# Kernel tuning notes

Hardware: AMD Instinct MI355X
Metric: run time of the kernel (lower is better)

Reference implementation:

```python
import jax, jax.numpy as jnp
import numpy as np

B, T, C = 8, 2048, 1024
HS, HO = 64, 64  # head_size, head_output_dim

def setup_inputs() -> dict:
    key = jax.random.key(0)
    k1, k2, k3, k4 = jax.random.split(key, 4)
    x = jax.random.normal(k1, (B, T, C), dtype=jnp.float32)
    Wk = jax.random.normal(k2, (HS, C), dtype=jnp.float32) * (C ** -0.5)
    Wq = jax.random.normal(k3, (HS, C), dtype=jnp.float32) * (C ** -0.5)
    Wv = jax.random.normal(k4, (HO, C), dtype=jnp.float32) * (C ** -0.5)
    return {"x": x, "Wk": Wk, "Wq": Wq, "Wv": Wv}

def reference(x, Wk, Wq, Wv):
    Bx, Tx, Cx = x.shape
    k = jnp.einsum('btc,hc->bth', x, Wk)  # [B,T,HS]
    q = jnp.einsum('btc,hc->bth', x, Wq)  # [B,T,HS]
    v = jnp.einsum('btc,oc->bto', x, Wv)  # [B,T,HO]
    scores = jnp.einsum('bth,bsh->bts', q, k)  # [B,T,T]
    causal = jnp.tril(jnp.ones((Tx, Tx), dtype=bool))
    scores = jnp.where(causal, scores, -jnp.inf)
    # original scales AFTER masking; -inf * scale stays -inf, same softmax result
    weights = jax.nn.softmax(scores * (HS ** -0.5), axis=-1)
    return jnp.einsum('bts,bso->bto', weights, v)
```

## Files before the change

### kernel.cpp

```cpp
#include <hip/hip_runtime.h>
#include <hip/hip_bf16.h>

typedef __attribute__((ext_vector_type(8))) short short8;
typedef __attribute__((ext_vector_type(4))) float float4v;

#define LOG2E 1.44269504088896340736f

typedef __attribute__((address_space(1))) const unsigned int gu32;
typedef __attribute__((address_space(3))) unsigned int su32;

__device__ __forceinline__ unsigned short f2bf(float f) {
    unsigned int u = __float_as_uint(f);
    unsigned int r = (u + 0x7fffu + ((u >> 16) & 1u)) >> 16;
    return (unsigned short)r;
}

__global__ void wconv_kernel(const float* __restrict__ Wk, const float* __restrict__ Wq,
                             const float* __restrict__ Wv, unsigned short* __restrict__ Wb) {
    int i = blockIdx.x * 256 + threadIdx.x;
    if (i >= 192 * 1024) return;
    float v;
    if (i < 65536)       v = Wk[i];
    else if (i < 131072) v = Wq[i - 65536];
    else                 v = Wv[i - 131072];
    Wb[i] = f2bf(v);
}

__global__ __launch_bounds__(256) void proj_kernel(
    const float* __restrict__ x, const unsigned short* __restrict__ Wb,
    unsigned short* __restrict__ qs, unsigned short* __restrict__ ks,
    unsigned short* __restrict__ vT) {
    __shared__ unsigned short Bl[2][12288];

    const int tid  = threadIdx.x;
    const int lane = tid & 63;
    const int wave = tid >> 6;
    const int rg   = wave & 1;
    const int g    = wave >> 1;
    const int quad = lane >> 4;
    const int l16  = lane & 15;
    const int t0   = blockIdx.x * 32;

    const int srow_in = lane >> 3;
    const int csrc    = (lane & 7) ^ srow_in;

    const int rowA = t0 + rg * 16 + l16;
    const float* xr = x + (size_t)rowA * 1024;

    float4v acc[6];
#pragma unroll
    for (int n = 0; n < 6; n++) acc[n] = (float4v){0.f, 0.f, 0.f, 0.f};

#define STAGE_B(BUF, KN)                                                          \
    {                                                                             \
        _Pragma("unroll")                                                         \
        for (int i = 0; i < 6; i++) {                                             \
            const int region = wave * 6 + i;                                      \
            const int rowg   = region * 8 + srow_in;                              \
            const unsigned short* src = Wb + (size_t)rowg * 1024 + (KN) + csrc * 8; \
            __builtin_amdgcn_global_load_lds((gu32*)src,                          \
                                             (su32*)&Bl[BUF][region * 512],       \
                                             16, 0, 0);                           \
        }                                                                         \
    }

    STAGE_B(0, 0)
    float4v areg[4];
    areg[0] = *(const float4v*)(xr + quad * 8);
    areg[1] = *(const float4v*)(xr + quad * 8 + 4);
    areg[2] = *(const float4v*)(xr + 32 + quad * 8);
    areg[3] = *(const float4v*)(xr + 32 + quad * 8 + 4);

    const int swz = l16 & 7;

#pragma unroll 2
    for (int kt = 0; kt < 16; kt++) {
        __syncthreads();
        const int kn = ((kt + 1) & 15) * 64;
        STAGE_B((kt + 1) & 1, kn)
        float4v anext[4];
        anext[0] = *(const float4v*)(xr + kn + quad * 8);
        anext[1] = *(const float4v*)(xr + kn + quad * 8 + 4);
        anext[2] = *(const float4v*)(xr + kn + 32 + quad * 8);
        anext[3] = *(const float4v*)(xr + kn + 32 + quad * 8 + 4);
        const unsigned short* Bc = Bl[kt & 1];
#pragma unroll
        for (int kc = 0; kc < 2; kc++) {
            short8 af;
#pragma unroll
            for (int j = 0; j < 4; j++) af[j] = (short)f2bf(areg[kc * 2][j]);
#pragma unroll
            for (int j = 0; j < 4; j++) af[4 + j] = (short)f2bf(areg[kc * 2 + 1][j]);
#pragma unroll
            for (int n = 0; n < 6; n++) {
                const int row  = (g * 6 + n) * 16 + l16;
                const int coff = ((kc * 4 + quad) ^ swz) * 8;
                const short8 bf = *(const short8*)&Bc[row * 64 + coff];
                acc[n] = __builtin_amdgcn_mfma_f32_16x16x32_bf16(af, bf, acc[n], 0, 0, 0);
            }
        }
#pragma unroll
        for (int i = 0; i < 4; i++) areg[i] = anext[i];
    }
#undef STAGE_B

    const int rowD = t0 + rg * 16 + quad * 4;
#pragma unroll
    for (int r = 0; r < 4; r++) {
        const int t = rowD + r;
        const int b = t >> 11, tt = t & 2047;
        if (g == 0) {
#pragma unroll
            for (int n = 0; n < 4; n++)
                ks[(size_t)t * 64 + n * 16 + l16] = f2bf(acc[n][r]);
#pragma unroll
            for (int n = 4; n < 6; n++)
                qs[(size_t)t * 64 + (n - 4) * 16 + l16] = f2bf(acc[n][r] * 0.125f);
        } else {
#pragma unroll
            for (int n = 0; n < 2; n++)
                qs[(size_t)t * 64 + (n + 2) * 16 + l16] = f2bf(acc[n][r] * 0.125f);
#pragma unroll
            for (int n = 2; n < 6; n++)
                vT[(size_t)b * 131072 + (size_t)((n - 2) * 16 + l16) * 2048 + tt] = f2bf(acc[n][r]);
        }
    }
}

__global__ __launch_bounds__(256) void attn_kernel(
    const unsigned short* __restrict__ qs, const unsigned short* __restrict__ ks,
    const unsigned short* __restrict__ vT, float* __restrict__ out) {
    __shared__ unsigned short Kl[4 * 64 * 72];
    __shared__ unsigned short Vl[64 * 264];
    __shared__ unsigned short P[4][16 * 72];
    __shared__ float Ll[4][16];
    float* Of = (float*)Kl;

    const int tid  = threadIdx.x;
    const int lane = tid & 63;
    const int wave = tid >> 6;
    const int quad = lane >> 4;
    const int l16  = lane & 15;
    const int bx   = blockIdx.x;
    const int b    = bx & 7;
    const int i    = bx >> 3;
    const int qt   = (i & 1) ? (127 - (i >> 1)) : (i >> 1);
    const int t0   = qt * 16;

    const unsigned short* qb = qs + (size_t)b * 131072;
    const unsigned short* kb = ks + (size_t)b * 131072;
    const unsigned short* vb = vT + (size_t)b * 131072;

    const int ksr = tid >> 3;
    const int ksc = (tid & 7) * 8;
    const int vsr = tid >> 5;
    const int vsc = (tid & 31) * 8;

    const int qrow = t0 + l16;
    const short8 qf0 = *(const short8*)(qb + (size_t)qrow * 64 + quad * 8);
    const short8 qf1 = *(const short8*)(qb + (size_t)qrow * 64 + 32 + quad * 8);

    float4v o[4];
#pragma unroll
    for (int ot = 0; ot < 4; ot++) o[ot] = (float4v){0.f, 0.f, 0.f, 0.f};
    float lpart = 0.f;

    const int nkb  = (qt >> 2) + 1;
    const int nsup = (nkb + 3) >> 2;

    for (int s = 0; s < nsup; s++) {
        const int key0 = s * 256;
        __syncthreads();
#pragma unroll
        for (int i2 = 0; i2 < 8; i2++) {
            int kr = key0 + i2 * 32 + ksr; kr = kr < 2047 ? kr : 2047;
            *(short8*)&Kl[(i2 * 32 + ksr) * 72 + ksc] = *(const short8*)(kb + (size_t)kr * 64 + ksc);
        }
#pragma unroll
        for (int i2 = 0; i2 < 8; i2++) {
            const int orow = i2 * 8 + vsr;
            int kc2 = key0 + vsc; kc2 = kc2 < 2040 ? kc2 : 2040;
            *(short8*)&Vl[orow * 264 + vsc] = *(const short8*)(vb + (size_t)orow * 2048 + kc2);
        }
        __syncthreads();

        const int jt = s * 4 + wave;
        if (jt < nkb) {
            const int kbase = wave * 64;
            float4v sv[4];
#pragma unroll
            for (int kt = 0; kt < 4; kt++) {
                const short8 ka = *(const short8*)&Kl[(kbase + kt * 16 + l16) * 72 + quad * 8];
                const short8 kc = *(const short8*)&Kl[(kbase + kt * 16 + l16) * 72 + 32 + quad * 8];
                float4v z = (float4v){0.f, 0.f, 0.f, 0.f};
                z = __builtin_amdgcn_mfma_f32_16x16x32_bf16(ka, qf0, z, 0, 0, 0);
                sv[kt] = __builtin_amdgcn_mfma_f32_16x16x32_bf16(kc, qf1, z, 0, 0, 0);
            }
            if (jt == nkb - 1) {
#pragma unroll
                for (int kt = 0; kt < 4; kt++)
#pragma unroll
                    for (int r = 0; r < 4; r++)
                        if (jt * 64 + kt * 16 + quad * 4 + r > qrow) sv[kt][r] = -1e30f;
            }
#pragma unroll
            for (int kt = 0; kt < 4; kt++) {
                float p0 = exp2f(sv[kt][0] * LOG2E);
                float p1 = exp2f(sv[kt][1] * LOG2E);
                float p2 = exp2f(sv[kt][2] * LOG2E);
                float p3 = exp2f(sv[kt][3] * LOG2E);
                lpart += (p0 + p1) + (p2 + p3);
                unsigned int lo = (unsigned int)f2bf(p0) | ((unsigned int)f2bf(p1) << 16);
                unsigned int hi = (unsigned int)f2bf(p2) | ((unsigned int)f2bf(p3) << 16);
                unsigned long long w = ((unsigned long long)hi << 32) | lo;
                *(unsigned long long*)&P[wave][l16 * 72 + kt * 16 + quad * 4] = w;
            }
#pragma unroll
            for (int kc = 0; kc < 2; kc++) {
                const short8 pf = *(const short8*)&P[wave][l16 * 72 + kc * 32 + quad * 8];
#pragma unroll
                for (int ot = 0; ot < 4; ot++) {
                    const short8 vf = *(const short8*)&Vl[(ot * 16 + l16) * 264 + wave * 64 + kc * 32 + quad * 8];
                    o[ot] = __builtin_amdgcn_mfma_f32_16x16x32_bf16(pf, vf, o[ot], 0, 0, 0);
                }
            }
        }
    }

    lpart += __shfl_xor(lpart, 16);
    lpart += __shfl_xor(lpart, 32);
    __syncthreads();
#pragma unroll
    for (int r = 0; r < 4; r++)
#pragma unroll
        for (int ot = 0; ot < 4; ot++)
            Of[wave * 1088 + (quad * 4 + r) * 68 + ot * 16 + l16] = o[ot][r];
    if (lane < 16) Ll[wave][lane] = lpart;
    __syncthreads();

    {
        const int row = tid >> 4;
        const int c0  = (tid & 15) * 4;
        const float lsum = Ll[0][row] + Ll[1][row] + Ll[2][row] + Ll[3][row];
        float4v v0 = *(const float4v*)&Of[0 * 1088 + row * 68 + c0];
        float4v v1 = *(const float4v*)&Of[1 * 1088 + row * 68 + c0];
        float4v v2 = *(const float4v*)&Of[2 * 1088 + row * 68 + c0];
        float4v v3 = *(const float4v*)&Of[3 * 1088 + row * 68 + c0];
        float4v res;
        const float inv = 1.0f / lsum;
#pragma unroll
        for (int j = 0; j < 4; j++)
            res[j] = ((v0[j] + v1[j]) + (v2[j] + v3[j])) * inv;
        float* ob = out + (size_t)b * 131072 + (size_t)(t0 + row) * 64 + c0;
        *(float4v*)ob = res;
    }
}

extern "C" void kernel_launch(void* const* d_in, const int* in_sizes, int n_in,
                              void* d_out, int out_size, void* d_ws, size_t ws_size,
                              hipStream_t stream) {
    const float* x  = (const float*)d_in[0];
    const float* Wk = (const float*)d_in[1];
    const float* Wq = (const float*)d_in[2];
    const float* Wv = (const float*)d_in[3];
    float* out = (float*)d_out;

    unsigned short* Wb  = (unsigned short*)d_ws;
    unsigned short* qsb = (unsigned short*)((char*)d_ws + 393216);
    unsigned short* ksb = qsb + 1048576;
    unsigned short* vTb = ksb + 1048576;

    hipLaunchKernelGGL(wconv_kernel, dim3(768), dim3(256), 0, stream, Wk, Wq, Wv, Wb);
    hipLaunchKernelGGL(proj_kernel, dim3(512), dim3(256), 0, stream, x, Wb, qsb, ksb, vTb);
    hipLaunchKernelGGL(attn_kernel, dim3(1024), dim3(256), 0, stream, qsb, ksb, vTb, out);
}
```

Baseline: 152.7 us.

## Drop LDS staging in projection kernel, load weights directly from global

Rewrites the QKV projection kernel so each block handles 16 rows instead of 32 and each wave reads its three weight tiles straight from global memory (L2-resident) rather than staging them through double-buffered LDS with barriers. It also deepens x prefetching to two k-steps ahead and doubles the grid to 1024 blocks with a launch-bounds occupancy hint. The aim is to remove __syncthreads and LDS traffic and to raise occupancy. The cost is more global/L2 weight reads, because the weights are re-read by twice as many blocks and are no longer shared across waves through LDS.

```diff
diff --git a/kernel.cpp b/kernel.cpp
--- a/kernel.cpp
+++ b/kernel.cpp
@@ -5,9 +5,6 @@
 typedef __attribute__((ext_vector_type(4))) float float4v;
 
 #define LOG2E 1.44269504088896340736f
-
-typedef __attribute__((address_space(1))) const unsigned int gu32;
-typedef __attribute__((address_space(3))) unsigned int su32;
 
 __device__ __forceinline__ unsigned short f2bf(float f) {
     unsigned int u = __float_as_uint(f);
@@ -26,103 +23,97 @@
     Wb[i] = f2bf(v);
 }
 
-__global__ __launch_bounds__(256) void proj_kernel(
+__global__ __launch_bounds__(256, 4) void proj_kernel(
     const float* __restrict__ x, const unsigned short* __restrict__ Wb,
     unsigned short* __restrict__ qs, unsigned short* __restrict__ ks,
     unsigned short* __restrict__ vT) {
-    __shared__ unsigned short Bl[2][12288];
-
     const int tid  = threadIdx.x;
     const int lane = tid & 63;
     const int wave = tid >> 6;
-    const int rg   = wave & 1;
-    const int g    = wave >> 1;
     const int quad = lane >> 4;
     const int l16  = lane & 15;
-    const int t0   = blockIdx.x * 32;
-
-    const int srow_in = lane >> 3;
-    const int csrc    = (lane & 7) ^ srow_in;
-
-    const int rowA = t0 + rg * 16 + l16;
-    const float* xr = x + (size_t)rowA * 1024;
-
-    float4v acc[6];
-#pragma unroll
-    for (int n = 0; n < 6; n++) acc[n] = (float4v){0.f, 0.f, 0.f, 0.f};
-
-#define STAGE_B(BUF, KN)                                                          \
-    {                                                                             \
-        _Pragma("unroll")                                                         \
-        for (int i = 0; i < 6; i++) {                                             \
-            const int region = wave * 6 + i;                                      \
-            const int rowg   = region * 8 + srow_in;                              \
-            const unsigned short* src = Wb + (size_t)rowg * 1024 + (KN) + csrc * 8; \
-            __builtin_amdgcn_global_load_lds((gu32*)src,                          \
-                                             (su32*)&Bl[BUF][region * 512],       \
-                                             16, 0, 0);                           \
-        }                                                                         \
-    }
-
-    STAGE_B(0, 0)
-    float4v areg[4];
-    areg[0] = *(const float4v*)(xr + quad * 8);
-    areg[1] = *(const float4v*)(xr + quad * 8 + 4);
-    areg[2] = *(const float4v*)(xr + 32 + quad * 8);
-    areg[3] = *(const float4v*)(xr + 32 + quad * 8 + 4);
-
-    const int swz = l16 & 7;
+    const int t0   = blockIdx.x * 16;
+
+    const float* xr = x + (size_t)(t0 + l16) * 1024;
+
+    const unsigned short* brow0 = Wb + (size_t)((wave * 3 + 0) * 16 + l16) * 1024 + quad * 8;
+    const unsigned short* brow1 = brow0 + 16 * 1024;
+    const unsigned short* brow2 = brow0 + 32 * 1024;
+
+    float4v acc0 = (float4v){0.f, 0.f, 0.f, 0.f};
+    float4v acc1 = (float4v){0.f, 0.f, 0.f, 0.f};
+    float4v acc2 = (float4v){0.f, 0.f, 0.f, 0.f};
+
+    float4v a0[4], a1[4];
+    a0[0] = *(const float4v*)(xr + quad * 8);
+    a0[1] = *(const float4v*)(xr + quad * 8 + 4);
+    a0[2] = *(const float4v*)(xr + 32 + quad * 8);
+    a0[3] = *(const float4v*)(xr + 32 + quad * 8 + 4);
+    a1[0] = *(const float4v*)(xr + 64 + quad * 8);
+    a1[1] = *(const float4v*)(xr + 64 + quad * 8 + 4);
+    a1[2] = *(const float4v*)(xr + 96 + quad * 8);
+    a1[3] = *(const float4v*)(xr + 96 + quad * 8 + 4);
 
 #pragma unroll 2
     for (int kt = 0; kt < 16; kt++) {
-        __syncthreads();
-        const int kn = ((kt + 1) & 15) * 64;
-        STAGE_B((kt + 1) & 1, kn)
-        float4v anext[4];
-        anext[0] = *(const float4v*)(xr + kn + quad * 8);
-        anext[1] = *(const float4v*)(xr + kn + quad * 8 + 4);
-        anext[2] = *(const float4v*)(xr + kn + 32 + quad * 8);
-        anext[3] = *(const float4v*)(xr + kn + 32 + quad * 8 + 4);
-        const unsigned short* Bc = Bl[kt & 1];
-#pragma unroll
-        for (int kc = 0; kc < 2; kc++) {
+        const int kn = ((kt + 2) & 15) * 64;
+        float4v an[4];
+        an[0] = *(const float4v*)(xr + kn + quad * 8);
+        an[1] = *(const float4v*)(xr + kn + quad * 8 + 4);
+        an[2] = *(const float4v*)(xr + kn + 32 + quad * 8);
+        an[3] = *(const float4v*)(xr + kn + 32 + quad * 8 + 4);
+
+        const unsigned short* b0 = brow0 + kt * 64;
+        const unsigned short* b1 = brow1 + kt * 64;
+        const unsigned short* b2 = brow2 + kt * 64;
+        const short8 bf00 = *(const short8*)(b0);
+        const short8 bf01 = *(const short8*)(b1);
+        const short8 bf02 = *(const short8*)(b2);
+        const short8 bf10 = *(const short8*)(b0 + 32);
+        const short8 bf11 = *(const short8*)(b1 + 32);
+        const short8 bf12 = *(const short8*)(b2 + 32);
+
+        {
             short8 af;
 #pragma unroll
-            for (int j = 0; j < 4; j++) af[j] = (short)f2bf(areg[kc * 2][j]);
-#pragma unroll
-            for (int j = 0; j < 4; j++) af[4 + j] = (short)f2bf(areg[kc * 2 + 1][j]);
-#pragma unroll
-            for (int n = 0; n < 6; n++) {
-                const int row  = (g * 6 + n) * 16 + l16;
-                const int coff = ((kc * 4 + quad) ^ swz) * 8;
-                const short8 bf = *(const short8*)&Bc[row * 64 + coff];
-                acc[n] = __builtin_amdgcn_mfma_f32_16x16x32_bf16(af, bf, acc[n], 0, 0, 0);
-            }
-        }
-#pragma unroll
-        for (int i = 0; i < 4; i++) areg[i] = anext[i];
-    }
-#undef STAGE_B
-
-    const int rowD = t0 + rg * 16 + quad * 4;
-#pragma unroll
-    for (int r = 0; r < 4; r++) {
-        const int t = rowD + r;
-        const int b = t >> 11, tt = t & 2047;
-        if (g == 0) {
-#pragma unroll
-            for (int n = 0; n < 4; n++)
-                ks[(size_t)t * 64 + n * 16 + l16] = f2bf(acc[n][r]);
-#pragma unroll
-            for (int n = 4; n < 6; n++)
-                qs[(size_t)t * 64 + (n - 4) * 16 + l16] = f2bf(acc[n][r] * 0.125f);
-        } else {
-#pragma unroll
-            for (int n = 0; n < 2; n++)
-                qs[(size_t)t * 64 + (n + 2) * 16 + l16] = f2bf(acc[n][r] * 0.125f);
-#pragma unroll
-            for (int n = 2; n < 6; n++)
-                vT[(size_t)b * 131072 + (size_t)((n - 2) * 16 + l16) * 2048 + tt] = f2bf(acc[n][r]);
+            for (int j = 0; j < 4; j++) af[j] = (short)f2bf(a0[0][j]);
+#pragma unroll
+            for (int j = 0; j < 4; j++) af[4 + j] = (short)f2bf(a0[1][j]);
+            acc0 = __builtin_amdgcn_mfma_f32_16x16x32_bf16(af, bf00, acc0, 0, 0, 0);
+            acc1 = __builtin_amdgcn_mfma_f32_16x16x32_bf16(af, bf01, acc1, 0, 0, 0);
+            acc2 = __builtin_amdgcn_mfma_f32_16x16x32_bf16(af, bf02, acc2, 0, 0, 0);
+        }
+        {
+            short8 af;
+#pragma unroll
+            for (int j = 0; j < 4; j++) af[j] = (short)f2bf(a0[2][j]);
+#pragma unroll
+            for (int j = 0; j < 4; j++) af[4 + j] = (short)f2bf(a0[3][j]);
+            acc0 = __builtin_amdgcn_mfma_f32_16x16x32_bf16(af, bf10, acc0, 0, 0, 0);
+            acc1 = __builtin_amdgcn_mfma_f32_16x16x32_bf16(af, bf11, acc1, 0, 0, 0);
+            acc2 = __builtin_amdgcn_mfma_f32_16x16x32_bf16(af, bf12, acc2, 0, 0, 0);
+        }
+#pragma unroll
+        for (int i = 0; i < 4; i++) { a0[i] = a1[i]; a1[i] = an[i]; }
+    }
+
+    const int rowD = t0 + quad * 4;
+    const float4v accs[3] = {acc0, acc1, acc2};
+#pragma unroll
+    for (int n = 0; n < 3; n++) {
+        const int mt = wave * 3 + n;
+#pragma unroll
+        for (int r = 0; r < 4; r++) {
+            const int t = rowD + r;
+            const float val = accs[n][r];
+            if (mt < 4) {
+                ks[(size_t)t * 64 + mt * 16 + l16] = f2bf(val);
+            } else if (mt < 8) {
+                qs[(size_t)t * 64 + (mt - 4) * 16 + l16] = f2bf(val * 0.125f);
+            } else {
+                const int b = t >> 11, tt = t & 2047;
+                vT[(size_t)b * 131072 + (size_t)((mt - 8) * 16 + l16) * 2048 + tt] = f2bf(val);
+            }
         }
     }
 }
@@ -271,6 +262,6 @@
     unsigned short* vTb = ksb + 1048576;
 
     hipLaunchKernelGGL(wconv_kernel, dim3(768), dim3(256), 0, stream, Wk, Wq, Wv, Wb);
-    hipLaunchKernelGGL(proj_kernel, dim3(512), dim3(256), 0, stream, x, Wb, qsb, ksb, vTb);
+    hipLaunchKernelGGL(proj_kernel, dim3(1024), dim3(256), 0, stream, x, Wb, qsb, ksb, vTb);
     hipLaunchKernelGGL(attn_kernel, dim3(1024), dim3(256), 0, stream, qsb, ksb, vTb, out);
 }
```

After: 195.5 us. +28.0%, slower.

## Deepen QKV projection pipeline with two-ahead A prefetch and explicit vmcnt waits

Applied to the files above, without the earlier changes.

Rewrites the K-loop of the QKV projection kernel so x rows are prefetched two tiles ahead instead of one, and fully unrolls the loop. It replaces __syncthreads with a manual s_waitcnt vmcnt(4) plus s_barrier, so the barrier waits only for the older loads and not the newest A prefetch. The aim is to hide global-load latency behind MFMA work. In exchange it uses more registers, and the hand-counted vmcnt must match the number of outstanding loads exactly or the code is incorrect.

```diff
diff --git a/kernel.cpp b/kernel.cpp
--- a/kernel.cpp
+++ b/kernel.cpp
@@ -65,32 +65,45 @@
     }
 
     STAGE_B(0, 0)
-    float4v areg[4];
-    areg[0] = *(const float4v*)(xr + quad * 8);
-    areg[1] = *(const float4v*)(xr + quad * 8 + 4);
-    areg[2] = *(const float4v*)(xr + 32 + quad * 8);
-    areg[3] = *(const float4v*)(xr + 32 + quad * 8 + 4);
+    float4v a0[4], a1[4];
+    a0[0] = *(const float4v*)(xr + quad * 8);
+    a0[1] = *(const float4v*)(xr + quad * 8 + 4);
+    a0[2] = *(const float4v*)(xr + 32 + quad * 8);
+    a0[3] = *(const float4v*)(xr + 32 + quad * 8 + 4);
+    a1[0] = *(const float4v*)(xr + 64 + quad * 8);
+    a1[1] = *(const float4v*)(xr + 64 + quad * 8 + 4);
+    a1[2] = *(const float4v*)(xr + 96 + quad * 8);
+    a1[3] = *(const float4v*)(xr + 96 + quad * 8 + 4);
 
     const int swz = l16 & 7;
 
-#pragma unroll 2
+#pragma unroll
     for (int kt = 0; kt < 16; kt++) {
-        __syncthreads();
-        const int kn = ((kt + 1) & 15) * 64;
-        STAGE_B((kt + 1) & 1, kn)
-        float4v anext[4];
-        anext[0] = *(const float4v*)(xr + kn + quad * 8);
-        anext[1] = *(const float4v*)(xr + kn + quad * 8 + 4);
-        anext[2] = *(const float4v*)(xr + kn + 32 + quad * 8);
-        anext[3] = *(const float4v*)(xr + kn + 32 + quad * 8 + 4);
+        __builtin_amdgcn_sched_barrier(0);
+        if (kt < 15) {
+            asm volatile("s_waitcnt vmcnt(4)" ::: "memory");
+        } else {
+            asm volatile("s_waitcnt vmcnt(0)" ::: "memory");
+        }
+        __builtin_amdgcn_s_barrier();
+        if (kt < 15) STAGE_B((kt + 1) & 1, (kt + 1) * 64)
+        asm volatile("" ::: "memory");
+        float4v an[4];
+        if (kt < 14) {
+            const int kn2 = (kt + 2) * 64;
+            an[0] = *(const float4v*)(xr + kn2 + quad * 8);
+            an[1] = *(const float4v*)(xr + kn2 + quad * 8 + 4);
+            an[2] = *(const float4v*)(xr + kn2 + 32 + quad * 8);
+            an[3] = *(const float4v*)(xr + kn2 + 32 + quad * 8 + 4);
+        }
         const unsigned short* Bc = Bl[kt & 1];
 #pragma unroll
         for (int kc = 0; kc < 2; kc++) {
             short8 af;
 #pragma unroll
-            for (int j = 0; j < 4; j++) af[j] = (short)f2bf(areg[kc * 2][j]);
-#pragma unroll
-            for (int j = 0; j < 4; j++) af[4 + j] = (short)f2bf(areg[kc * 2 + 1][j]);
+            for (int j = 0; j < 4; j++) af[j] = (short)f2bf(a0[kc * 2][j]);
+#pragma unroll
+            for (int j = 0; j < 4; j++) af[4 + j] = (short)f2bf(a0[kc * 2 + 1][j]);
 #pragma unroll
             for (int n = 0; n < 6; n++) {
                 const int row  = (g * 6 + n) * 16 + l16;
@@ -99,8 +112,13 @@
                 acc[n] = __builtin_amdgcn_mfma_f32_16x16x32_bf16(af, bf, acc[n], 0, 0, 0);
             }
         }
-#pragma unroll
-        for (int i = 0; i < 4; i++) areg[i] = anext[i];
+        if (kt < 14) {
+#pragma unroll
+            for (int i = 0; i < 4; i++) { a0[i] = a1[i]; a1[i] = an[i]; }
+        } else if (kt < 15) {
+#pragma unroll
+            for (int i = 0; i < 4; i++) a0[i] = a1[i];
+        }
     }
 #undef STAGE_B
 
```

Result: no change. 150.0 us (-1.8%).
